# Performance work log

Measured on AMD Instinct MI355X. Metric: run time of the kernel, lower is better.

The kernel has to match this reference:

```python
import jax, jax.numpy as jnp
import numpy as np
from functools import reduce
from jax.scipy.linalg import block_diag

M = 3          # ancilla / layered-matrix qubits
NQ = 4         # QNN qubits
L = 8          # num_qnn_layers
NOUT = 4       # number of QNN blocks
DIM_A = 2 ** M   # 8
DIM_Q = 2 ** NQ  # 16
BATCH = 131072


def _ry(t):
    # RY rotation: [[cos(t/2), -sin(t/2)], [sin(t/2), cos(t/2)]]
    c = jnp.cos(t * 0.5)
    s = jnp.sin(t * 0.5)
    return jnp.stack([jnp.stack([c, -s]), jnp.stack([s, c])])


def _cnot_full(n, c, t):
    # dense CNOT on n qubits (control c, target t), built once as a constant
    dim = 2 ** n
    P = np.zeros((dim, dim), np.float32)
    for i in range(dim):
        bits = [(i >> (n - 1 - k)) & 1 for k in range(n)]
        if bits[c] == 1:
            bits[t] ^= 1
        j = sum(b << (n - 1 - k) for k, b in enumerate(bits))
        P[j, i] = 1.0
    return jnp.asarray(P)

# entangling layer: CNOT(0,1) then CNOT(1,2) then CNOT(2,3) -> matrix product in reverse
_ENT = reduce(lambda acc, g: g @ acc, [_cnot_full(NQ, q, q + 1) for q in range(NQ - 1)], jnp.eye(DIM_Q))


def _build_qnn(thetas):  # thetas: (L, NQ) -> 16x16 unitary
    U = jnp.eye(DIM_Q)
    for l in range(L):
        rys = reduce(jnp.kron, [_ry(thetas[l, q]) for q in range(NQ)])
        U = _ENT @ (rys @ U)
    return U


def _layered_product_matrix(alpha):
    # hierarchical tree of RY blocks: layer l has 2^l rotations, block-diagonal,
    # kron'd with identity on the remaining qubits; product over layers.
    U = jnp.eye(DIM_A)
    idx = 0
    for l in range(M):
        nb = 2 ** l
        bd = block_diag(*[_ry(alpha[idx + b]) for b in range(nb)])
        idx += nb
        U = jnp.kron(bd, jnp.eye(2 ** (M - l - 1))) @ U
    return U


def setup_inputs() -> dict:
    key = jax.random.key(0)
    k1, k2, k3 = jax.random.split(key, 3)
    x = jax.random.uniform(k1, (BATCH, 4), dtype=jnp.float32)
    alpha = jax.random.uniform(k2, (2 ** M - 1,), dtype=jnp.float32) * 6.28
    qnn_thetas = jax.random.uniform(k3, (NOUT, L * NQ), dtype=jnp.float32) * 6.28
    return {"x": x, "alpha": alpha, "qnn_thetas": qnn_thetas}


def reference(x, alpha, qnn_thetas):
    b = x.shape[0]
    ang = x * (np.pi / 0.5)  # (b, 4)
    c = jnp.cos(ang * 0.5)
    s = jnp.sin(ang * 0.5)
    # per-qubit RY|0> amplitudes -> encoding state = kron of the four 2-vectors
    v = [jnp.stack([c[:, q], s[:, q]], axis=1) for q in range(NQ)]
    enc = jnp.einsum('bi,bj,bk,bl->bijkl', *v).reshape(b, DIM_Q)  # (b, 16)
    ent0 = _layered_product_matrix(alpha)[:, 0]                    # (8,) = U_ent |0>
    inter = ent0[None, :, None] * enc[:, None, :]                  # (b, 8, 16) = kron state
    qnn = [_build_qnn(qnn_thetas[j].reshape(L, NQ)) for j in range(NOUT)]
    blocks = jnp.stack(qnn + [jnp.eye(DIM_Q)] * (DIM_A - NOUT))    # (8, 16, 16) block-diagonal
    fin = jnp.einsum('kij,bkj->bki', blocks, inter)                # (b, 8, 16)
    # measure Z on qubits 3,4,5 (first three QNN qubits)
    p = (fin * fin).reshape(b, DIM_A, 2, 2, 2, 2)
    z = jnp.array([1.0, -1.0], dtype=x.dtype)
    e3 = jnp.einsum('bkijlm,i->b', p, z)
    e4 = jnp.einsum('bkijlm,j->b', p, z)
    e5 = jnp.einsum('bkijlm,l->b', p, z)
    return (jnp.stack([e3, e4, e5], axis=1) + 1.0) * 0.5           # (b, 3)
```

## Files before the change

### kernel.cpp

```cpp
#include <hip/hip_runtime.h>

#define NQ 4
#define DIMQ 16
#define NLAY 8
#define NOUT 4
#define NPAIR 136
#define TPB 256
#define SPT 2

__global__ __launch_bounds__(TPB) void qnn_fused(const float4* __restrict__ x,
                                                 const float* __restrict__ alpha,
                                                 const float* __restrict__ thetas,
                                                 float* __restrict__ out,
                                                 int batch, int nthreads) {
    __shared__ float2 csT[128];
    __shared__ float2 csA[8];
    __shared__ float  U[NOUT][DIMQ][DIMQ];
    __shared__ float  w[8];
    __shared__ float  Af[3][DIMQ][DIMQ];
    __shared__ float  Mf[3][10][12];

    const int tid = threadIdx.x;

    if (tid < 128) {
        const float t = thetas[tid] * 0.5f;
        csT[tid] = make_float2(cosf(t), sinf(t));
    } else if (tid < 135) {
        const float t = alpha[tid - 128] * 0.5f;
        csA[tid - 128] = make_float2(cosf(t), sinf(t));
    }
    __syncthreads();

    if (tid < 64) {
        const int k = tid >> 4, col = tid & 15;
        float st[16];
        #pragma unroll
        for (int i = 0; i < 16; ++i) st[i] = (i == col) ? 1.0f : 0.0f;
        #pragma unroll 1
        for (int l = 0; l < NLAY; ++l) {
            #pragma unroll
            for (int q = 0; q < NQ; ++q) {
                const float2 cs = csT[k * 32 + l * 4 + q];
                const float c = cs.x, s = cs.y;
                const int pb = 1 << (3 - q);
                #pragma unroll
                for (int i0 = 0; i0 < 16; ++i0) {
                    if (i0 & pb) continue;
                    const int i1 = i0 | pb;
                    const float a0 = st[i0], a1 = st[i1];
                    st[i0] = c * a0 - s * a1;
                    st[i1] = s * a0 + c * a1;
                }
            }
            #pragma unroll
            for (int q = 0; q < NQ - 1; ++q) {
                const int cb = 1 << (3 - q), tb = 1 << (2 - q);
                #pragma unroll
                for (int i = 0; i < 16; ++i) {
                    if ((i & cb) && !(i & tb)) {
                        const int j = i | tb;
                        const float tmp = st[i]; st[i] = st[j]; st[j] = tmp;
                    }
                }
            }
        }
        #pragma unroll
        for (int r = 0; r < 16; ++r) U[k][col][r] = st[r];
    }
    if (tid == 64) {
        float e[8];
        #pragma unroll
        for (int i = 0; i < 8; ++i) e[i] = (i == 0) ? 1.0f : 0.0f;
        int idx = 0;
        #pragma unroll
        for (int l = 0; l < 3; ++l) {
            const int p = 2 - l, pb = 1 << p;
            #pragma unroll
            for (int i0 = 0; i0 < 8; ++i0) {
                if (i0 & pb) continue;
                const int i1 = i0 | pb;
                const float2 cs = csA[idx + (i0 >> (p + 1))];
                const float a0 = e[i0], a1 = e[i1];
                e[i0] = cs.x * a0 - cs.y * a1;
                e[i1] = cs.y * a0 + cs.x * a1;
            }
            idx += (1 << l);
        }
        for (int k = 0; k < 4; ++k) w[k] = e[k] * e[k];
        w[4] = e[4]*e[4] + e[5]*e[5] + e[6]*e[6] + e[7]*e[7];
    }
    __syncthreads();

    for (int j = tid; j < NPAIR; j += TPB) {
        int r = j, t = 0;
        while (r >= 16 - t) { r -= 16 - t; ++t; }
        const int u = t + r;
        float gs[8] = {0,0,0,0,0,0,0,0};
        #pragma unroll
        for (int k = 0; k < NOUT; ++k) {
            #pragma unroll
            for (int rr = 0; rr < 16; ++rr)
                gs[rr >> 1] = fmaf(w[k], U[k][t][rr] * U[k][u][rr], gs[rr >> 1]);
        }
        float A0 = 0.f, A1 = 0.f, A2 = 0.f;
        #pragma unroll
        for (int c = 0; c < 8; ++c) {
            A0 += (c & 4) ? -gs[c] : gs[c];
            A1 += (c & 2) ? -gs[c] : gs[c];
            A2 += (c & 1) ? -gs[c] : gs[c];
        }
        if (t == u) {
            A0 += ((t >> 3) & 1) ? -w[4] : w[4];
            A1 += ((t >> 2) & 1) ? -w[4] : w[4];
            A2 += ((t >> 1) & 1) ? -w[4] : w[4];
        }
        Af[0][t][u] = A0; Af[0][u][t] = A0;
        Af[1][t][u] = A1; Af[1][u][t] = A1;
        Af[2][t][u] = A2; Af[2][u][t] = A2;
    }
    __syncthreads();

    for (int e = tid; e < 360; e += TPB) {
        const int m = e / 120, r = e - m * 120, p = r / 12, q = r - p * 12;
        float v = 0.0f;
        if (q < 10) {
            int i, k, jj, ll;
            if (p < 4)      { i = 0; k = p; }
            else if (p < 7) { i = 1; k = p - 3; }
            else if (p < 9) { i = 2; k = p - 5; }
            else            { i = 3; k = 3; }
            if (q < 4)      { jj = 0; ll = q; }
            else if (q < 7) { jj = 1; ll = q - 3; }
            else if (q < 9) { jj = 2; ll = q - 5; }
            else            { jj = 3; ll = 3; }
            if (i < k && jj < ll)       v = Af[m][4*i+jj][4*k+ll] + Af[m][4*i+ll][4*k+jj];
            else if (i == k && jj < ll) v = Af[m][4*i+jj][4*i+ll];
            else if (i < k && jj == ll) v = Af[m][4*i+jj][4*k+jj];
            else                        v = 0.5f * Af[m][4*i+jj][4*i+jj];
        }
        Mf[m][p][q] = v;
    }
    __syncthreads();

    const int gid = blockIdx.x * TPB + tid;
    float G01[SPT][10], G23[SPT][12], acc[SPT][3];
    #pragma unroll
    for (int s = 0; s < SPT; ++s) {
        const int b = gid + s * nthreads;
        const float4 xv = (b < batch) ? x[b] : make_float4(0.f, 0.f, 0.f, 0.f);
        float c0, s0, c1, s1, c2, s2, c3, s3;
        sincospif(xv.x, &s0, &c0);
        sincospif(xv.y, &s1, &c1);
        sincospif(xv.z, &s2, &c2);
        sincospif(xv.w, &s3, &c3);
        float f01[4], f23[4];
        f01[0] = c0 * c1; f01[1] = c0 * s1; f01[2] = s0 * c1; f01[3] = s0 * s1;
        f23[0] = c2 * c3; f23[1] = c2 * s3; f23[2] = s2 * c3; f23[3] = s2 * s3;
        int idx = 0;
        #pragma unroll
        for (int i = 0; i < 4; ++i)
            #pragma unroll
            for (int k = i; k < 4; ++k) G01[s][idx++] = f01[i] * f01[k];
        idx = 0;
        #pragma unroll
        for (int j = 0; j < 4; ++j)
            #pragma unroll
            for (int l = j; l < 4; ++l) G23[s][idx++] = f23[j] * f23[l];
        G23[s][10] = 0.f; G23[s][11] = 0.f;
        acc[s][0] = 0.5f; acc[s][1] = 0.5f; acc[s][2] = 0.5f;
    }

    #pragma unroll
    for (int m = 0; m < 3; ++m) {
        #pragma unroll
        for (int p = 0; p < 10; ++p) {
            const float4* row = (const float4*)&Mf[m][p][0];
            const float4 r0 = row[0], r1 = row[1], r2 = row[2];
            #pragma unroll
            for (int s = 0; s < SPT; ++s) {
                float z;
                z = r0.x * G23[s][0];
                z = fmaf(r0.y, G23[s][1], z);
                z = fmaf(r0.z, G23[s][2], z);
                z = fmaf(r0.w, G23[s][3], z);
                z = fmaf(r1.x, G23[s][4], z);
                z = fmaf(r1.y, G23[s][5], z);
                z = fmaf(r1.z, G23[s][6], z);
                z = fmaf(r1.w, G23[s][7], z);
                z = fmaf(r2.x, G23[s][8], z);
                z = fmaf(r2.y, G23[s][9], z);
                acc[s][m] = fmaf(G01[s][p], z, acc[s][m]);
            }
        }
    }

    #pragma unroll
    for (int s = 0; s < SPT; ++s) {
        const int b = gid + s * nthreads;
        if (b < batch) {
            out[b * 3 + 0] = acc[s][0];
            out[b * 3 + 1] = acc[s][1];
            out[b * 3 + 2] = acc[s][2];
        }
    }
}

extern "C" void kernel_launch(void* const* d_in, const int* in_sizes, int n_in,
                              void* d_out, int out_size, void* d_ws, size_t ws_size,
                              hipStream_t stream) {
    const float* x      = (const float*)d_in[0];
    const float* alpha  = (const float*)d_in[1];
    const float* thetas = (const float*)d_in[2];

    const int batch = in_sizes[0] / 4;
    const int blocks = (batch + TPB * SPT - 1) / (TPB * SPT);
    const int nthreads = blocks * TPB;
    qnn_fused<<<blocks, TPB, 0, stream>>>((const float4*)x, alpha, thetas,
                                          (float*)d_out, batch, nthreads);
}
```

Baseline: 14.58 us.

## Split per-block redundant unitary setup into a one-block setup kernel plus main kernel

Before, every block rebuilt the four QNN unitaries and the quadratic-form matrices in shared memory. Now a single-block setup kernel computes the 300-element matrix once into workspace, and a lean main kernel with one sample per thread reads it through uniform global loads. This removes redundant per-block setup and syncs. In exchange it adds a second launch serialized after a single-threaded-heavy setup block, and the main kernel drops the two-samples-per-thread amortization of the matrix loads.

```diff
diff --git a/kernel.cpp b/kernel.cpp
--- a/kernel.cpp
+++ b/kernel.cpp
@@ -5,20 +5,15 @@
 #define NLAY 8
 #define NOUT 4
 #define NPAIR 136
-#define TPB 256
-#define SPT 2
-
-__global__ __launch_bounds__(TPB) void qnn_fused(const float4* __restrict__ x,
-                                                 const float* __restrict__ alpha,
+
+__global__ __launch_bounds__(256) void qnn_setup(const float* __restrict__ alpha,
                                                  const float* __restrict__ thetas,
-                                                 float* __restrict__ out,
-                                                 int batch, int nthreads) {
+                                                 float* __restrict__ M_out) {
     __shared__ float2 csT[128];
     __shared__ float2 csA[8];
     __shared__ float  U[NOUT][DIMQ][DIMQ];
     __shared__ float  w[8];
     __shared__ float  Af[3][DIMQ][DIMQ];
-    __shared__ float  Mf[3][10][12];
 
     const int tid = threadIdx.x;
 
@@ -41,15 +36,14 @@
             #pragma unroll
             for (int q = 0; q < NQ; ++q) {
                 const float2 cs = csT[k * 32 + l * 4 + q];
-                const float c = cs.x, s = cs.y;
                 const int pb = 1 << (3 - q);
                 #pragma unroll
                 for (int i0 = 0; i0 < 16; ++i0) {
                     if (i0 & pb) continue;
                     const int i1 = i0 | pb;
                     const float a0 = st[i0], a1 = st[i1];
-                    st[i0] = c * a0 - s * a1;
-                    st[i1] = s * a0 + c * a1;
+                    st[i0] = cs.x * a0 - cs.y * a1;
+                    st[i1] = cs.y * a0 + cs.x * a1;
                 }
             }
             #pragma unroll
@@ -91,7 +85,7 @@
     }
     __syncthreads();
 
-    for (int j = tid; j < NPAIR; j += TPB) {
+    for (int j = tid; j < NPAIR; j += 256) {
         int r = j, t = 0;
         while (r >= 16 - t) { r -= 16 - t; ++t; }
         const int u = t + r;
@@ -120,89 +114,78 @@
     }
     __syncthreads();
 
-    for (int e = tid; e < 360; e += TPB) {
-        const int m = e / 120, r = e - m * 120, p = r / 12, q = r - p * 12;
-        float v = 0.0f;
-        if (q < 10) {
-            int i, k, jj, ll;
-            if (p < 4)      { i = 0; k = p; }
-            else if (p < 7) { i = 1; k = p - 3; }
-            else if (p < 9) { i = 2; k = p - 5; }
-            else            { i = 3; k = 3; }
-            if (q < 4)      { jj = 0; ll = q; }
-            else if (q < 7) { jj = 1; ll = q - 3; }
-            else if (q < 9) { jj = 2; ll = q - 5; }
-            else            { jj = 3; ll = 3; }
-            if (i < k && jj < ll)       v = Af[m][4*i+jj][4*k+ll] + Af[m][4*i+ll][4*k+jj];
-            else if (i == k && jj < ll) v = Af[m][4*i+jj][4*i+ll];
-            else if (i < k && jj == ll) v = Af[m][4*i+jj][4*k+jj];
-            else                        v = 0.5f * Af[m][4*i+jj][4*i+jj];
-        }
-        Mf[m][p][q] = v;
-    }
-    __syncthreads();
-
-    const int gid = blockIdx.x * TPB + tid;
-    float G01[SPT][10], G23[SPT][12], acc[SPT][3];
+    for (int e = tid; e < 300; e += 256) {
+        const int m = e / 100, r = e - m * 100, p = r / 10, q = r - p * 10;
+        int i, k, jj, ll;
+        if (p < 4)      { i = 0; k = p; }
+        else if (p < 7) { i = 1; k = p - 3; }
+        else if (p < 9) { i = 2; k = p - 5; }
+        else            { i = 3; k = 3; }
+        if (q < 4)      { jj = 0; ll = q; }
+        else if (q < 7) { jj = 1; ll = q - 3; }
+        else if (q < 9) { jj = 2; ll = q - 5; }
+        else            { jj = 3; ll = 3; }
+        float v;
+        if (i < k && jj < ll)       v = Af[m][4*i+jj][4*k+ll] + Af[m][4*i+ll][4*k+jj];
+        else if (i == k && jj < ll) v = Af[m][4*i+jj][4*i+ll];
+        else if (i < k && jj == ll) v = Af[m][4*i+jj][4*k+jj];
+        else                        v = 0.5f * Af[m][4*i+jj][4*i+jj];
+        M_out[e] = v;
+    }
+}
+
+__global__ __launch_bounds__(256) void qnn_main(const float4* __restrict__ x,
+                                                const float* __restrict__ M,
+                                                float* __restrict__ out,
+                                                int batch) {
+    const int b = blockIdx.x * 256 + threadIdx.x;
+    if (b >= batch) return;
+
+    const float4 xv = x[b];
+    float c0, s0, c1, s1, c2, s2, c3, s3;
+    sincospif(xv.x, &s0, &c0);
+    sincospif(xv.y, &s1, &c1);
+    sincospif(xv.z, &s2, &c2);
+    sincospif(xv.w, &s3, &c3);
+
+    float f01[4], f23[4];
+    f01[0] = c0 * c1; f01[1] = c0 * s1; f01[2] = s0 * c1; f01[3] = s0 * s1;
+    f23[0] = c2 * c3; f23[1] = c2 * s3; f23[2] = s2 * c3; f23[3] = s2 * s3;
+
+    float G01[10], G23[10];
+    {
+        int idx = 0;
+        #pragma unroll
+        for (int i = 0; i < 4; ++i)
+            #pragma unroll
+            for (int k = i; k < 4; ++k) { G01[idx] = f01[i] * f01[k]; ++idx; }
+        idx = 0;
+        #pragma unroll
+        for (int j = 0; j < 4; ++j)
+            #pragma unroll
+            for (int l = j; l < 4; ++l) { G23[idx] = f23[j] * f23[l]; ++idx; }
+    }
+
+    float acc0 = 0.5f, acc1 = 0.5f, acc2 = 0.5f;
     #pragma unroll
-    for (int s = 0; s < SPT; ++s) {
-        const int b = gid + s * nthreads;
-        const float4 xv = (b < batch) ? x[b] : make_float4(0.f, 0.f, 0.f, 0.f);
-        float c0, s0, c1, s1, c2, s2, c3, s3;
-        sincospif(xv.x, &s0, &c0);
-        sincospif(xv.y, &s1, &c1);
-        sincospif(xv.z, &s2, &c2);
-        sincospif(xv.w, &s3, &c3);
-        float f01[4], f23[4];
-        f01[0] = c0 * c1; f01[1] = c0 * s1; f01[2] = s0 * c1; f01[3] = s0 * s1;
-        f23[0] = c2 * c3; f23[1] = c2 * s3; f23[2] = s2 * c3; f23[3] = s2 * s3;
-        int idx = 0;
-        #pragma unroll
-        for (int i = 0; i < 4; ++i)
-            #pragma unroll
-            for (int k = i; k < 4; ++k) G01[s][idx++] = f01[i] * f01[k];
-        idx = 0;
-        #pragma unroll
-        for (int j = 0; j < 4; ++j)
-            #pragma unroll
-            for (int l = j; l < 4; ++l) G23[s][idx++] = f23[j] * f23[l];
-        G23[s][10] = 0.f; G23[s][11] = 0.f;
-        acc[s][0] = 0.5f; acc[s][1] = 0.5f; acc[s][2] = 0.5f;
-    }
-
-    #pragma unroll
-    for (int m = 0; m < 3; ++m) {
-        #pragma unroll
-        for (int p = 0; p < 10; ++p) {
-            const float4* row = (const float4*)&Mf[m][p][0];
-            const float4 r0 = row[0], r1 = row[1], r2 = row[2];
-            #pragma unroll
-            for (int s = 0; s < SPT; ++s) {
-                float z;
-                z = r0.x * G23[s][0];
-                z = fmaf(r0.y, G23[s][1], z);
-                z = fmaf(r0.z, G23[s][2], z);
-                z = fmaf(r0.w, G23[s][3], z);
-                z = fmaf(r1.x, G23[s][4], z);
-                z = fmaf(r1.y, G23[s][5], z);
-                z = fmaf(r1.z, G23[s][6], z);
-                z = fmaf(r1.w, G23[s][7], z);
-                z = fmaf(r2.x, G23[s][8], z);
-                z = fmaf(r2.y, G23[s][9], z);
-                acc[s][m] = fmaf(G01[s][p], z, acc[s][m]);
-            }
-        }
-    }
-
-    #pragma unroll
-    for (int s = 0; s < SPT; ++s) {
-        const int b = gid + s * nthreads;
-        if (b < batch) {
-            out[b * 3 + 0] = acc[s][0];
-            out[b * 3 + 1] = acc[s][1];
-            out[b * 3 + 2] = acc[s][2];
-        }
-    }
+    for (int p = 0; p < 10; ++p) {
+        float z0 = M[        p * 10] * G23[0];
+        float z1 = M[100 +   p * 10] * G23[0];
+        float z2 = M[200 +   p * 10] * G23[0];
+        #pragma unroll
+        for (int q = 1; q < 10; ++q) {
+            z0 = fmaf(M[        p * 10 + q], G23[q], z0);
+            z1 = fmaf(M[100 +   p * 10 + q], G23[q], z1);
+            z2 = fmaf(M[200 +   p * 10 + q], G23[q], z2);
+        }
+        acc0 = fmaf(G01[p], z0, acc0);
+        acc1 = fmaf(G01[p], z1, acc1);
+        acc2 = fmaf(G01[p], z2, acc2);
+    }
+
+    out[b * 3 + 0] = acc0;
+    out[b * 3 + 1] = acc1;
+    out[b * 3 + 2] = acc2;
 }
 
 extern "C" void kernel_launch(void* const* d_in, const int* in_sizes, int n_in,
@@ -211,10 +194,11 @@
     const float* x      = (const float*)d_in[0];
     const float* alpha  = (const float*)d_in[1];
     const float* thetas = (const float*)d_in[2];
+    float* M = (float*)d_ws;
+
+    qnn_setup<<<1, 256, 0, stream>>>(alpha, thetas, M);
 
     const int batch = in_sizes[0] / 4;
-    const int blocks = (batch + TPB * SPT - 1) / (TPB * SPT);
-    const int nthreads = blocks * TPB;
-    qnn_fused<<<blocks, TPB, 0, stream>>>((const float4*)x, alpha, thetas,
-                                          (float*)d_out, batch, nthreads);
+    const int blocks = (batch + 255) / 256;
+    qnn_main<<<blocks, 256, 0, stream>>>((const float4*)x, M, (float*)d_out, batch);
 }
```

After: 16.32 us. +12.0%, slower.

## Restructure kernel into single-wave blocks with 4 samples per lane

Applied to the files above, without the earlier changes.

Blocks shrink to one 64-lane wavefront, each handling 256 samples (4 per lane). The x loads are issued before the per-block setup so their latency overlaps the matrix construction. Each block still rebuilds the QNN unitaries, and now folds sqrt of the ancilla weights into U. The Gram-pair stage uses a 2x2-tiled register block over 36 lanes, and U rows are padded and read with float4. The aim is to cut per-block synchronisation cost and idle threads in the redundant setup, at the price of more blocks, each repeating that setup, and higher register pressure.

```diff
diff --git a/kernel.cpp b/kernel.cpp
--- a/kernel.cpp
+++ b/kernel.cpp
@@ -1,73 +1,42 @@
 #include <hip/hip_runtime.h>
 
-#define NQ 4
-#define DIMQ 16
 #define NLAY 8
-#define NOUT 4
-#define NPAIR 136
-#define TPB 256
-#define SPT 2
-
-__global__ __launch_bounds__(TPB) void qnn_fused(const float4* __restrict__ x,
-                                                 const float* __restrict__ alpha,
-                                                 const float* __restrict__ thetas,
-                                                 float* __restrict__ out,
-                                                 int batch, int nthreads) {
+
+__global__ __launch_bounds__(64) void qnn_wave(const float4* __restrict__ x,
+                                               const float* __restrict__ alpha,
+                                               const float* __restrict__ thetas,
+                                               float* __restrict__ out,
+                                               int batch) {
     __shared__ float2 csT[128];
     __shared__ float2 csA[8];
-    __shared__ float  U[NOUT][DIMQ][DIMQ];
-    __shared__ float  w[8];
-    __shared__ float  Af[3][DIMQ][DIMQ];
+    __shared__ float  U[4][16][20];
+    __shared__ float  Af[3][16][16];
     __shared__ float  Mf[3][10][12];
 
-    const int tid = threadIdx.x;
-
-    if (tid < 128) {
-        const float t = thetas[tid] * 0.5f;
-        csT[tid] = make_float2(cosf(t), sinf(t));
-    } else if (tid < 135) {
-        const float t = alpha[tid - 128] * 0.5f;
-        csA[tid - 128] = make_float2(cosf(t), sinf(t));
-    }
-    __syncthreads();
-
-    if (tid < 64) {
-        const int k = tid >> 4, col = tid & 15;
-        float st[16];
-        #pragma unroll
-        for (int i = 0; i < 16; ++i) st[i] = (i == col) ? 1.0f : 0.0f;
-        #pragma unroll 1
-        for (int l = 0; l < NLAY; ++l) {
-            #pragma unroll
-            for (int q = 0; q < NQ; ++q) {
-                const float2 cs = csT[k * 32 + l * 4 + q];
-                const float c = cs.x, s = cs.y;
-                const int pb = 1 << (3 - q);
-                #pragma unroll
-                for (int i0 = 0; i0 < 16; ++i0) {
-                    if (i0 & pb) continue;
-                    const int i1 = i0 | pb;
-                    const float a0 = st[i0], a1 = st[i1];
-                    st[i0] = c * a0 - s * a1;
-                    st[i1] = s * a0 + c * a1;
-                }
-            }
-            #pragma unroll
-            for (int q = 0; q < NQ - 1; ++q) {
-                const int cb = 1 << (3 - q), tb = 1 << (2 - q);
-                #pragma unroll
-                for (int i = 0; i < 16; ++i) {
-                    if ((i & cb) && !(i & tb)) {
-                        const int j = i | tb;
-                        const float tmp = st[i]; st[i] = st[j]; st[j] = tmp;
-                    }
-                }
-            }
-        }
-        #pragma unroll
-        for (int r = 0; r < 16; ++r) U[k][col][r] = st[r];
-    }
-    if (tid == 64) {
+    const int lane = threadIdx.x;
+    const int base = blockIdx.x * 256;
+
+    float4 xv[4];
+    #pragma unroll
+    for (int s = 0; s < 4; ++s) {
+        const int b = base + s * 64 + lane;
+        xv[s] = x[(b < batch) ? b : 0];
+    }
+
+    {
+        const float t0 = thetas[lane] * 0.5f;
+        const float t1 = thetas[64 + lane] * 0.5f;
+        csT[lane]      = make_float2(cosf(t0), sinf(t0));
+        csT[64 + lane] = make_float2(cosf(t1), sinf(t1));
+        if (lane < 7) {
+            const float ta = alpha[lane] * 0.5f;
+            csA[lane] = make_float2(cosf(ta), sinf(ta));
+        }
+    }
+    __syncthreads();
+
+    float w0, w1, w2, w3, w4;
+    {
         float e[8];
         #pragma unroll
         for (int i = 0; i < 8; ++i) e[i] = (i == 0) ? 1.0f : 0.0f;
@@ -86,73 +55,142 @@
             }
             idx += (1 << l);
         }
-        for (int k = 0; k < 4; ++k) w[k] = e[k] * e[k];
-        w[4] = e[4]*e[4] + e[5]*e[5] + e[6]*e[6] + e[7]*e[7];
-    }
-    __syncthreads();
-
-    for (int j = tid; j < NPAIR; j += TPB) {
-        int r = j, t = 0;
-        while (r >= 16 - t) { r -= 16 - t; ++t; }
-        const int u = t + r;
-        float gs[8] = {0,0,0,0,0,0,0,0};
-        #pragma unroll
-        for (int k = 0; k < NOUT; ++k) {
-            #pragma unroll
-            for (int rr = 0; rr < 16; ++rr)
-                gs[rr >> 1] = fmaf(w[k], U[k][t][rr] * U[k][u][rr], gs[rr >> 1]);
-        }
-        float A0 = 0.f, A1 = 0.f, A2 = 0.f;
-        #pragma unroll
-        for (int c = 0; c < 8; ++c) {
-            A0 += (c & 4) ? -gs[c] : gs[c];
-            A1 += (c & 2) ? -gs[c] : gs[c];
-            A2 += (c & 1) ? -gs[c] : gs[c];
-        }
-        if (t == u) {
-            A0 += ((t >> 3) & 1) ? -w[4] : w[4];
-            A1 += ((t >> 2) & 1) ? -w[4] : w[4];
-            A2 += ((t >> 1) & 1) ? -w[4] : w[4];
-        }
-        Af[0][t][u] = A0; Af[0][u][t] = A0;
-        Af[1][t][u] = A1; Af[1][u][t] = A1;
-        Af[2][t][u] = A2; Af[2][u][t] = A2;
-    }
-    __syncthreads();
-
-    for (int e = tid; e < 360; e += TPB) {
-        const int m = e / 120, r = e - m * 120, p = r / 12, q = r - p * 12;
-        float v = 0.0f;
-        if (q < 10) {
-            int i, k, jj, ll;
-            if (p < 4)      { i = 0; k = p; }
-            else if (p < 7) { i = 1; k = p - 3; }
-            else if (p < 9) { i = 2; k = p - 5; }
-            else            { i = 3; k = 3; }
-            if (q < 4)      { jj = 0; ll = q; }
-            else if (q < 7) { jj = 1; ll = q - 3; }
-            else if (q < 9) { jj = 2; ll = q - 5; }
-            else            { jj = 3; ll = 3; }
-            if (i < k && jj < ll)       v = Af[m][4*i+jj][4*k+ll] + Af[m][4*i+ll][4*k+jj];
-            else if (i == k && jj < ll) v = Af[m][4*i+jj][4*i+ll];
-            else if (i < k && jj == ll) v = Af[m][4*i+jj][4*k+jj];
-            else                        v = 0.5f * Af[m][4*i+jj][4*i+jj];
-        }
-        Mf[m][p][q] = v;
-    }
-    __syncthreads();
-
-    const int gid = blockIdx.x * TPB + tid;
-    float G01[SPT][10], G23[SPT][12], acc[SPT][3];
-    #pragma unroll
-    for (int s = 0; s < SPT; ++s) {
-        const int b = gid + s * nthreads;
-        const float4 xv = (b < batch) ? x[b] : make_float4(0.f, 0.f, 0.f, 0.f);
+        w0 = e[0]*e[0]; w1 = e[1]*e[1]; w2 = e[2]*e[2]; w3 = e[3]*e[3];
+        w4 = e[4]*e[4] + e[5]*e[5] + e[6]*e[6] + e[7]*e[7];
+    }
+
+    {
+        const int k = lane >> 4, col = lane & 15;
+        float st[16];
+        #pragma unroll
+        for (int i = 0; i < 16; ++i) st[i] = (i == col) ? 1.0f : 0.0f;
+        #pragma unroll 1
+        for (int l = 0; l < NLAY; ++l) {
+            #pragma unroll
+            for (int q = 0; q < 4; ++q) {
+                const float2 cs = csT[k * 32 + l * 4 + q];
+                const int pb = 1 << (3 - q);
+                #pragma unroll
+                for (int i0 = 0; i0 < 16; ++i0) {
+                    if (i0 & pb) continue;
+                    const int i1 = i0 | pb;
+                    const float a0 = st[i0], a1 = st[i1];
+                    st[i0] = cs.x * a0 - cs.y * a1;
+                    st[i1] = cs.y * a0 + cs.x * a1;
+                }
+            }
+            #pragma unroll
+            for (int q = 0; q < 3; ++q) {
+                const int cb = 1 << (3 - q), tb = 1 << (2 - q);
+                #pragma unroll
+                for (int i = 0; i < 16; ++i) {
+                    if ((i & cb) && !(i & tb)) {
+                        const int j = i | tb;
+                        const float tmp = st[i]; st[i] = st[j]; st[j] = tmp;
+                    }
+                }
+            }
+        }
+        const float sw = sqrtf((k == 0) ? w0 : (k == 1) ? w1 : (k == 2) ? w2 : w3);
+        float4* dst = (float4*)&U[k][col][0];
+        dst[0] = make_float4(st[0]*sw,  st[1]*sw,  st[2]*sw,  st[3]*sw);
+        dst[1] = make_float4(st[4]*sw,  st[5]*sw,  st[6]*sw,  st[7]*sw);
+        dst[2] = make_float4(st[8]*sw,  st[9]*sw,  st[10]*sw, st[11]*sw);
+        dst[3] = make_float4(st[12]*sw, st[13]*sw, st[14]*sw, st[15]*sw);
+    }
+    __syncthreads();
+
+    if (lane < 36) {
+        int r = lane, T = 0;
+        while (r >= 8 - T) { r -= 8 - T; ++T; }
+        const int V = T + r;
+
+        float gs[2][2][8] = {};
+        #pragma unroll
+        for (int k = 0; k < 4; ++k) {
+            float a[2][16], c[2][16];
+            #pragma unroll
+            for (int d = 0; d < 2; ++d) {
+                const float4* ct = (const float4*)&U[k][2*T + d][0];
+                const float4* cu = (const float4*)&U[k][2*V + d][0];
+                #pragma unroll
+                for (int v = 0; v < 4; ++v) {
+                    const float4 av = ct[v], cv = cu[v];
+                    a[d][4*v+0] = av.x; a[d][4*v+1] = av.y;
+                    a[d][4*v+2] = av.z; a[d][4*v+3] = av.w;
+                    c[d][4*v+0] = cv.x; c[d][4*v+1] = cv.y;
+                    c[d][4*v+2] = cv.z; c[d][4*v+3] = cv.w;
+                }
+            }
+            #pragma unroll
+            for (int dt = 0; dt < 2; ++dt)
+                #pragma unroll
+                for (int du = 0; du < 2; ++du)
+                    #pragma unroll
+                    for (int rr = 0; rr < 16; ++rr)
+                        gs[dt][du][rr >> 1] =
+                            fmaf(a[dt][rr], c[du][rr], gs[dt][du][rr >> 1]);
+        }
+        #pragma unroll
+        for (int dt = 0; dt < 2; ++dt) {
+            #pragma unroll
+            for (int du = 0; du < 2; ++du) {
+                const int t = 2*T + dt, u = 2*V + du;
+                float A0 = 0.f, A1 = 0.f, A2 = 0.f;
+                #pragma unroll
+                for (int cc = 0; cc < 8; ++cc) {
+                    const float g = gs[dt][du][cc];
+                    A0 += (cc & 4) ? -g : g;
+                    A1 += (cc & 2) ? -g : g;
+                    A2 += (cc & 1) ? -g : g;
+                }
+                if (t == u) {
+                    A0 += ((t >> 3) & 1) ? -w4 : w4;
+                    A1 += ((t >> 2) & 1) ? -w4 : w4;
+                    A2 += ((t >> 1) & 1) ? -w4 : w4;
+                }
+                Af[0][t][u] = A0; Af[0][u][t] = A0;
+                Af[1][t][u] = A1; Af[1][u][t] = A1;
+                Af[2][t][u] = A2; Af[2][u][t] = A2;
+            }
+        }
+    }
+    __syncthreads();
+
+    #pragma unroll 1
+    for (int round = 0; round < 6; ++round) {
+        const int e = round * 64 + lane;
+        if (e < 360) {
+            const int m = e / 120, rr = e - m * 120, p = rr / 12, q = rr - p * 12;
+            float v = 0.0f;
+            if (q < 10) {
+                int i, k, jj, ll;
+                if (p < 4)      { i = 0; k = p; }
+                else if (p < 7) { i = 1; k = p - 3; }
+                else if (p < 9) { i = 2; k = p - 5; }
+                else            { i = 3; k = 3; }
+                if (q < 4)      { jj = 0; ll = q; }
+                else if (q < 7) { jj = 1; ll = q - 3; }
+                else if (q < 9) { jj = 2; ll = q - 5; }
+                else            { jj = 3; ll = 3; }
+                if (i < k && jj < ll)       v = Af[m][4*i+jj][4*k+ll] + Af[m][4*i+ll][4*k+jj];
+                else if (i == k && jj < ll) v = Af[m][4*i+jj][4*i+ll];
+                else if (i < k && jj == ll) v = Af[m][4*i+jj][4*k+jj];
+                else                        v = 0.5f * Af[m][4*i+jj][4*i+jj];
+            }
+            Mf[m][p][q] = v;
+        }
+    }
+    __syncthreads();
+
+    float G01[4][10], G23[4][10], acc[4][3];
+    #pragma unroll
+    for (int s = 0; s < 4; ++s) {
         float c0, s0, c1, s1, c2, s2, c3, s3;
-        sincospif(xv.x, &s0, &c0);
-        sincospif(xv.y, &s1, &c1);
-        sincospif(xv.z, &s2, &c2);
-        sincospif(xv.w, &s3, &c3);
+        sincospif(xv[s].x, &s0, &c0);
+        sincospif(xv[s].y, &s1, &c1);
+        sincospif(xv[s].z, &s2, &c2);
+        sincospif(xv[s].w, &s3, &c3);
         float f01[4], f23[4];
         f01[0] = c0 * c1; f01[1] = c0 * s1; f01[2] = s0 * c1; f01[3] = s0 * s1;
         f23[0] = c2 * c3; f23[1] = c2 * s3; f23[2] = s2 * c3; f23[3] = s2 * s3;
@@ -160,13 +198,12 @@
         #pragma unroll
         for (int i = 0; i < 4; ++i)
             #pragma unroll
-            for (int k = i; k < 4; ++k) G01[s][idx++] = f01[i] * f01[k];
+            for (int k = i; k < 4; ++k) { G01[s][idx] = f01[i] * f01[k]; ++idx; }
         idx = 0;
         #pragma unroll
         for (int j = 0; j < 4; ++j)
             #pragma unroll
-            for (int l = j; l < 4; ++l) G23[s][idx++] = f23[j] * f23[l];
-        G23[s][10] = 0.f; G23[s][11] = 0.f;
+            for (int l = j; l < 4; ++l) { G23[s][idx] = f23[j] * f23[l]; ++idx; }
         acc[s][0] = 0.5f; acc[s][1] = 0.5f; acc[s][2] = 0.5f;
     }
 
@@ -177,7 +214,7 @@
             const float4* row = (const float4*)&Mf[m][p][0];
             const float4 r0 = row[0], r1 = row[1], r2 = row[2];
             #pragma unroll
-            for (int s = 0; s < SPT; ++s) {
+            for (int s = 0; s < 4; ++s) {
                 float z;
                 z = r0.x * G23[s][0];
                 z = fmaf(r0.y, G23[s][1], z);
@@ -195,8 +232,8 @@
     }
 
     #pragma unroll
-    for (int s = 0; s < SPT; ++s) {
-        const int b = gid + s * nthreads;
+    for (int s = 0; s < 4; ++s) {
+        const int b = base + s * 64 + lane;
         if (b < batch) {
             out[b * 3 + 0] = acc[s][0];
             out[b * 3 + 1] = acc[s][1];
@@ -213,8 +250,7 @@
     const float* thetas = (const float*)d_in[2];
 
     const int batch = in_sizes[0] / 4;
-    const int blocks = (batch + TPB * SPT - 1) / (TPB * SPT);
-    const int nthreads = blocks * TPB;
-    qnn_fused<<<blocks, TPB, 0, stream>>>((const float4*)x, alpha, thetas,
-                                          (float*)d_out, batch, nthreads);
+    const int blocks = (batch + 255) / 256;
+    qnn_wave<<<blocks, 64, 0, stream>>>((const float4*)x, alpha, thetas,
+                                        (float*)d_out, batch);
 }
```

Result: slower. 18.68 us (+28.1%).

## Prefetch x before setup, fold encoder weights into U, vectorize Gram build

Applied to the files above, without the earlier changes.

The per-sample x loads are issued at kernel entry so their global-memory latency overlaps the shared-memory setup phase. The ancilla amplitudes are now computed redundantly by each of the 64 QNN threads, which folds the weight into the stored unitary columns and removes a separate single-thread phase. U is padded to 20 floats per row and written and read as float4, which cuts LDS instructions in the pair-Gram step. The final contraction is interleaved across the three measurement channels for more ILP. The trade-off is higher register pressure from holding x across the setup and from the wider loop body.

```diff
diff --git a/kernel.cpp b/kernel.cpp
--- a/kernel.cpp
+++ b/kernel.cpp
@@ -1,10 +1,6 @@
 #include <hip/hip_runtime.h>
 
-#define NQ 4
-#define DIMQ 16
 #define NLAY 8
-#define NOUT 4
-#define NPAIR 136
 #define TPB 256
 #define SPT 2
 
@@ -15,12 +11,20 @@
                                                  int batch, int nthreads) {
     __shared__ float2 csT[128];
     __shared__ float2 csA[8];
-    __shared__ float  U[NOUT][DIMQ][DIMQ];
-    __shared__ float  w[8];
-    __shared__ float  Af[3][DIMQ][DIMQ];
+    __shared__ float  U[4][16][20];
+    __shared__ float  w4s;
+    __shared__ float  Af[3][16][16];
     __shared__ float  Mf[3][10][12];
 
     const int tid = threadIdx.x;
+    const int gid = blockIdx.x * TPB + tid;
+
+    float4 xv[SPT];
+    #pragma unroll
+    for (int s = 0; s < SPT; ++s) {
+        const int b = gid + s * nthreads;
+        xv[s] = x[(b < batch) ? b : 0];
+    }
 
     if (tid < 128) {
         const float t = thetas[tid] * 0.5f;
@@ -32,6 +36,27 @@
     __syncthreads();
 
     if (tid < 64) {
+        float e[8];
+        #pragma unroll
+        for (int i = 0; i < 8; ++i) e[i] = (i == 0) ? 1.0f : 0.0f;
+        int idx = 0;
+        #pragma unroll
+        for (int l = 0; l < 3; ++l) {
+            const int p = 2 - l, pb = 1 << p;
+            #pragma unroll
+            for (int i0 = 0; i0 < 8; ++i0) {
+                if (i0 & pb) continue;
+                const int i1 = i0 | pb;
+                const float2 cs = csA[idx + (i0 >> (p + 1))];
+                const float a0 = e[i0], a1 = e[i1];
+                e[i0] = cs.x * a0 - cs.y * a1;
+                e[i1] = cs.y * a0 + cs.x * a1;
+            }
+            idx += (1 << l);
+        }
+        if (tid == 0)
+            w4s = e[4]*e[4] + e[5]*e[5] + e[6]*e[6] + e[7]*e[7];
+
         const int k = tid >> 4, col = tid & 15;
         float st[16];
         #pragma unroll
@@ -39,21 +64,20 @@
         #pragma unroll 1
         for (int l = 0; l < NLAY; ++l) {
             #pragma unroll
-            for (int q = 0; q < NQ; ++q) {
+            for (int q = 0; q < 4; ++q) {
                 const float2 cs = csT[k * 32 + l * 4 + q];
-                const float c = cs.x, s = cs.y;
                 const int pb = 1 << (3 - q);
                 #pragma unroll
                 for (int i0 = 0; i0 < 16; ++i0) {
                     if (i0 & pb) continue;
                     const int i1 = i0 | pb;
                     const float a0 = st[i0], a1 = st[i1];
-                    st[i0] = c * a0 - s * a1;
-                    st[i1] = s * a0 + c * a1;
+                    st[i0] = cs.x * a0 - cs.y * a1;
+                    st[i1] = cs.y * a0 + cs.x * a1;
                 }
             }
             #pragma unroll
-            for (int q = 0; q < NQ - 1; ++q) {
+            for (int q = 0; q < 3; ++q) {
                 const int cb = 1 << (3 - q), tb = 1 << (2 - q);
                 #pragma unroll
                 for (int i = 0; i < 16; ++i) {
@@ -64,55 +88,49 @@
                 }
             }
         }
-        #pragma unroll
-        for (int r = 0; r < 16; ++r) U[k][col][r] = st[r];
-    }
-    if (tid == 64) {
-        float e[8];
-        #pragma unroll
-        for (int i = 0; i < 8; ++i) e[i] = (i == 0) ? 1.0f : 0.0f;
-        int idx = 0;
-        #pragma unroll
-        for (int l = 0; l < 3; ++l) {
-            const int p = 2 - l, pb = 1 << p;
-            #pragma unroll
-            for (int i0 = 0; i0 < 8; ++i0) {
-                if (i0 & pb) continue;
-                const int i1 = i0 | pb;
-                const float2 cs = csA[idx + (i0 >> (p + 1))];
-                const float a0 = e[i0], a1 = e[i1];
-                e[i0] = cs.x * a0 - cs.y * a1;
-                e[i1] = cs.y * a0 + cs.x * a1;
-            }
-            idx += (1 << l);
-        }
-        for (int k = 0; k < 4; ++k) w[k] = e[k] * e[k];
-        w[4] = e[4]*e[4] + e[5]*e[5] + e[6]*e[6] + e[7]*e[7];
-    }
-    __syncthreads();
-
-    for (int j = tid; j < NPAIR; j += TPB) {
-        int r = j, t = 0;
+        const float sw = e[k];
+        float4* dst = (float4*)&U[k][col][0];
+        dst[0] = make_float4(st[0]*sw,  st[1]*sw,  st[2]*sw,  st[3]*sw);
+        dst[1] = make_float4(st[4]*sw,  st[5]*sw,  st[6]*sw,  st[7]*sw);
+        dst[2] = make_float4(st[8]*sw,  st[9]*sw,  st[10]*sw, st[11]*sw);
+        dst[3] = make_float4(st[12]*sw, st[13]*sw, st[14]*sw, st[15]*sw);
+    }
+    __syncthreads();
+
+    if (tid < 136) {
+        int r = tid, t = 0;
         while (r >= 16 - t) { r -= 16 - t; ++t; }
         const int u = t + r;
+
         float gs[8] = {0,0,0,0,0,0,0,0};
         #pragma unroll
-        for (int k = 0; k < NOUT; ++k) {
-            #pragma unroll
-            for (int rr = 0; rr < 16; ++rr)
-                gs[rr >> 1] = fmaf(w[k], U[k][t][rr] * U[k][u][rr], gs[rr >> 1]);
+        for (int k = 0; k < 4; ++k) {
+            const float4* ct = (const float4*)&U[k][t][0];
+            const float4* cu = (const float4*)&U[k][u][0];
+            const float4 a0 = ct[0], a1 = ct[1], a2 = ct[2], a3 = ct[3];
+            const float4 c0 = cu[0], c1 = cu[1], c2 = cu[2], c3 = cu[3];
+            gs[0] = fmaf(a0.x, c0.x, gs[0]); gs[0] = fmaf(a0.y, c0.y, gs[0]);
+            gs[1] = fmaf(a0.z, c0.z, gs[1]); gs[1] = fmaf(a0.w, c0.w, gs[1]);
+            gs[2] = fmaf(a1.x, c1.x, gs[2]); gs[2] = fmaf(a1.y, c1.y, gs[2]);
+            gs[3] = fmaf(a1.z, c1.z, gs[3]); gs[3] = fmaf(a1.w, c1.w, gs[3]);
+            gs[4] = fmaf(a2.x, c2.x, gs[4]); gs[4] = fmaf(a2.y, c2.y, gs[4]);
+            gs[5] = fmaf(a2.z, c2.z, gs[5]); gs[5] = fmaf(a2.w, c2.w, gs[5]);
+            gs[6] = fmaf(a3.x, c3.x, gs[6]); gs[6] = fmaf(a3.y, c3.y, gs[6]);
+            gs[7] = fmaf(a3.z, c3.z, gs[7]); gs[7] = fmaf(a3.w, c3.w, gs[7]);
         }
         float A0 = 0.f, A1 = 0.f, A2 = 0.f;
         #pragma unroll
         for (int c = 0; c < 8; ++c) {
-            A0 += (c & 4) ? -gs[c] : gs[c];
-            A1 += (c & 2) ? -gs[c] : gs[c];
-            A2 += (c & 1) ? -gs[c] : gs[c];
+            const float g = gs[c];
+            A0 += (c & 4) ? -g : g;
+            A1 += (c & 2) ? -g : g;
+            A2 += (c & 1) ? -g : g;
         }
         if (t == u) {
-            A0 += ((t >> 3) & 1) ? -w[4] : w[4];
-            A1 += ((t >> 2) & 1) ? -w[4] : w[4];
-            A2 += ((t >> 1) & 1) ? -w[4] : w[4];
+            const float w4 = w4s;
+            A0 += ((t >> 3) & 1) ? -w4 : w4;
+            A1 += ((t >> 2) & 1) ? -w4 : w4;
+            A2 += ((t >> 1) & 1) ? -w4 : w4;
         }
         Af[0][t][u] = A0; Af[0][u][t] = A0;
         Af[1][t][u] = A1; Af[1][u][t] = A1;
@@ -121,7 +139,7 @@
     __syncthreads();
 
     for (int e = tid; e < 360; e += TPB) {
-        const int m = e / 120, r = e - m * 120, p = r / 12, q = r - p * 12;
+        const int m = e / 120, rr = e - m * 120, p = rr / 12, q = rr - p * 12;
         float v = 0.0f;
         if (q < 10) {
             int i, k, jj, ll;
@@ -142,17 +160,14 @@
     }
     __syncthreads();
 
-    const int gid = blockIdx.x * TPB + tid;
-    float G01[SPT][10], G23[SPT][12], acc[SPT][3];
+    float G01[SPT][10], G23[SPT][10], acc[SPT][3];
     #pragma unroll
     for (int s = 0; s < SPT; ++s) {
-        const int b = gid + s * nthreads;
-        const float4 xv = (b < batch) ? x[b] : make_float4(0.f, 0.f, 0.f, 0.f);
         float c0, s0, c1, s1, c2, s2, c3, s3;
-        sincospif(xv.x, &s0, &c0);
-        sincospif(xv.y, &s1, &c1);
-        sincospif(xv.z, &s2, &c2);
-        sincospif(xv.w, &s3, &c3);
+        sincospif(xv[s].x, &s0, &c0);
+        sincospif(xv[s].y, &s1, &c1);
+        sincospif(xv[s].z, &s2, &c2);
+        sincospif(xv[s].w, &s3, &c3);
         float f01[4], f23[4];
         f01[0] = c0 * c1; f01[1] = c0 * s1; f01[2] = s0 * c1; f01[3] = s0 * s1;
         f23[0] = c2 * c3; f23[1] = c2 * s3; f23[2] = s2 * c3; f23[3] = s2 * s3;
@@ -160,37 +175,62 @@
         #pragma unroll
         for (int i = 0; i < 4; ++i)
             #pragma unroll
-            for (int k = i; k < 4; ++k) G01[s][idx++] = f01[i] * f01[k];
+            for (int k = i; k < 4; ++k) { G01[s][idx] = f01[i] * f01[k]; ++idx; }
         idx = 0;
         #pragma unroll
         for (int j = 0; j < 4; ++j)
             #pragma unroll
-            for (int l = j; l < 4; ++l) G23[s][idx++] = f23[j] * f23[l];
-        G23[s][10] = 0.f; G23[s][11] = 0.f;
+            for (int l = j; l < 4; ++l) { G23[s][idx] = f23[j] * f23[l]; ++idx; }
         acc[s][0] = 0.5f; acc[s][1] = 0.5f; acc[s][2] = 0.5f;
     }
 
     #pragma unroll
-    for (int m = 0; m < 3; ++m) {
-        #pragma unroll
-        for (int p = 0; p < 10; ++p) {
-            const float4* row = (const float4*)&Mf[m][p][0];
-            const float4 r0 = row[0], r1 = row[1], r2 = row[2];
-            #pragma unroll
-            for (int s = 0; s < SPT; ++s) {
-                float z;
-                z = r0.x * G23[s][0];
-                z = fmaf(r0.y, G23[s][1], z);
-                z = fmaf(r0.z, G23[s][2], z);
-                z = fmaf(r0.w, G23[s][3], z);
-                z = fmaf(r1.x, G23[s][4], z);
-                z = fmaf(r1.y, G23[s][5], z);
-                z = fmaf(r1.z, G23[s][6], z);
-                z = fmaf(r1.w, G23[s][7], z);
-                z = fmaf(r2.x, G23[s][8], z);
-                z = fmaf(r2.y, G23[s][9], z);
-                acc[s][m] = fmaf(G01[s][p], z, acc[s][m]);
-            }
+    for (int p = 0; p < 10; ++p) {
+        const float4 m00 = *(const float4*)&Mf[0][p][0];
+        const float4 m01 = *(const float4*)&Mf[0][p][4];
+        const float4 m02 = *(const float4*)&Mf[0][p][8];
+        const float4 m10 = *(const float4*)&Mf[1][p][0];
+        const float4 m11 = *(const float4*)&Mf[1][p][4];
+        const float4 m12 = *(const float4*)&Mf[1][p][8];
+        const float4 m20 = *(const float4*)&Mf[2][p][0];
+        const float4 m21 = *(const float4*)&Mf[2][p][4];
+        const float4 m22 = *(const float4*)&Mf[2][p][8];
+        #pragma unroll
+        for (int s = 0; s < SPT; ++s) {
+            float z0, z1, z2;
+            z0 = m00.x * G23[s][0];
+            z1 = m10.x * G23[s][0];
+            z2 = m20.x * G23[s][0];
+            z0 = fmaf(m00.y, G23[s][1], z0);
+            z1 = fmaf(m10.y, G23[s][1], z1);
+            z2 = fmaf(m20.y, G23[s][1], z2);
+            z0 = fmaf(m00.z, G23[s][2], z0);
+            z1 = fmaf(m10.z, G23[s][2], z1);
+            z2 = fmaf(m20.z, G23[s][2], z2);
+            z0 = fmaf(m00.w, G23[s][3], z0);
+            z1 = fmaf(m10.w, G23[s][3], z1);
+            z2 = fmaf(m20.w, G23[s][3], z2);
+            z0 = fmaf(m01.x, G23[s][4], z0);
+            z1 = fmaf(m11.x, G23[s][4], z1);
+            z2 = fmaf(m21.x, G23[s][4], z2);
+            z0 = fmaf(m01.y, G23[s][5], z0);
+            z1 = fmaf(m11.y, G23[s][5], z1);
+            z2 = fmaf(m21.y, G23[s][5], z2);
+            z0 = fmaf(m01.z, G23[s][6], z0);
+            z1 = fmaf(m11.z, G23[s][6], z1);
+            z2 = fmaf(m21.z, G23[s][6], z2);
+            z0 = fmaf(m01.w, G23[s][7], z0);
+            z1 = fmaf(m11.w, G23[s][7], z1);
+            z2 = fmaf(m21.w, G23[s][7], z2);
+            z0 = fmaf(m02.x, G23[s][8], z0);
+            z1 = fmaf(m12.x, G23[s][8], z1);
+            z2 = fmaf(m22.x, G23[s][8], z2);
+            z0 = fmaf(m02.y, G23[s][9], z0);
+            z1 = fmaf(m12.y, G23[s][9], z1);
+            z2 = fmaf(m22.y, G23[s][9], z2);
+            acc[s][0] = fmaf(G01[s][p], z0, acc[s][0]);
+            acc[s][1] = fmaf(G01[s][p], z1, acc[s][1]);
+            acc[s][2] = fmaf(G01[s][p], z2, acc[s][2]);
         }
     }
 
```

Measured after the change: 14.32 us. No clear change (-1.8%).
